# Kernel tuning notes

Measured on AMD Instinct MI355X. Metric: run time of the kernel, lower is better.

## Reference

```python
import jax, jax.numpy as jnp
import numpy as np

KERNEL = 3
BN_EPS = 1e-5


def setup_inputs() -> dict:
    key = jax.random.key(0)
    ks = jax.random.split(key, 4)
    B, C, H, W = 32, 256, 64, 64
    x = jax.random.normal(ks[0], (B, C, H, W), dtype=jnp.float32)
    conv_w = jax.random.normal(ks[1], (KERNEL * C, C), dtype=jnp.float32) * (1.0 / np.sqrt(C))
    bn_weight = jnp.ones((KERNEL * C,), dtype=jnp.float32)
    bn_bias = jnp.zeros((KERNEL * C,), dtype=jnp.float32)
    bn_mean = jnp.zeros((KERNEL * C,), dtype=jnp.float32)
    bn_var = jnp.ones((KERNEL * C,), dtype=jnp.float32)
    gamma = jax.random.normal(ks[2], (C, 1, 1), dtype=jnp.float32)
    beta = jnp.ones((C, 1, 1), dtype=jnp.float32)
    return {"x": x, "conv_w": conv_w, "bn_weight": bn_weight, "bn_bias": bn_bias,
            "bn_mean": bn_mean, "bn_var": bn_var, "gamma": gamma, "beta": beta}


def reference(x, conv_w, bn_weight, bn_bias, bn_mean, bn_var, gamma, beta):
    # x: (B, C, H, W)
    B, C, H, W = x.shape
    K = KERNEL
    # Filter generation: GAP -> 1x1 conv -> BN (inference stats) -> tanh
    g = x.mean(axis=(2, 3))                      # (B, C)
    y = jnp.einsum('bc,kc->bk', g, conv_w)       # (B, K*C)
    y = (y - bn_mean) * jax.lax.rsqrt(bn_var + BN_EPS) * bn_weight + bn_bias
    f = jnp.tanh(y).reshape(B, K, C)             # (B, K, C), tap k for channel c
    # Dynamic per-channel local filter along the CHANNEL axis with reflect pad.
    # Equivalent to the unfold path: out[b,c,h,w] = sum_k f[b,k,c] * x[b, reflect(c+k-1), h, w]
    xp = jnp.pad(x, ((0, 0), (K // 2, K // 2), (0, 0), (0, 0)), mode='reflect')
    out = f[:, 0, :, None, None] * xp[:, 0:C]
    for k in range(1, K):
        out = out + f[:, k, :, None, None] * xp[:, k:k + C]
    return out * gamma + x * beta
```

## Files before the change

### kernel.cpp

```cpp
#include <hip/hip_runtime.h>

#define NC 256
#define NB 32
#define HW 4096
#define HW4 1024
#define KC 768
#define BN_EPS 1e-5f
#define CG 32

typedef float f32x4 __attribute__((ext_vector_type(4)));

__global__ __launch_bounds__(256) void gap_kernel(const float* __restrict__ x,
                                                  float* __restrict__ g) {
    const int bc = blockIdx.x;
    const f32x4* xp = reinterpret_cast<const f32x4*>(x) + (size_t)bc * HW4;
    const int t = threadIdx.x;
    float s = 0.f;
#pragma unroll
    for (int k = 0; k < 4; ++k) {
        f32x4 v = xp[t + k * 256];
        s += (v.x + v.y) + (v.z + v.w);
    }
#pragma unroll
    for (int off = 32; off > 0; off >>= 1) s += __shfl_down(s, off, 64);
    __shared__ float warp_sums[4];
    const int lane = t & 63, w = t >> 6;
    if (lane == 0) warp_sums[w] = s;
    __syncthreads();
    if (t == 0) {
        float tot = (warp_sums[0] + warp_sums[1]) + (warp_sums[2] + warp_sums[3]);
        g[bc] = tot * (1.0f / HW);
    }
}

__global__ __launch_bounds__(256) void filt_kernel(const float* __restrict__ g,
                                                   const float* __restrict__ cw,
                                                   const float* __restrict__ bn_w,
                                                   const float* __restrict__ bn_b,
                                                   const float* __restrict__ bn_m,
                                                   const float* __restrict__ bn_v,
                                                   float* __restrict__ f) {
    const int b = blockIdx.y;
    const int t = threadIdx.x;
    __shared__ float gs[NC];
    gs[t] = g[b * NC + t];
    __syncthreads();
    const int wave = t >> 6, lane = t & 63;
    const f32x4 gv = reinterpret_cast<const f32x4*>(gs)[lane];
    const int row0 = blockIdx.x * 32 + wave * 8;
#pragma unroll
    for (int i = 0; i < 8; ++i) {
        const int j = row0 + i;
        const f32x4 wv = reinterpret_cast<const f32x4*>(cw + (size_t)j * NC)[lane];
        float s = fmaf(gv.x, wv.x, fmaf(gv.y, wv.y, fmaf(gv.z, wv.z, gv.w * wv.w)));
#pragma unroll
        for (int off = 32; off > 0; off >>= 1) s += __shfl_down(s, off, 64);
        if (lane == 0) {
            float yn = (s - bn_m[j]) * rsqrtf(bn_v[j] + BN_EPS) * bn_w[j] + bn_b[j];
            f[b * KC + j] = tanhf(yn);
        }
    }
}

__global__ __launch_bounds__(256) void apply_kernel(const float* __restrict__ x,
                                                    const float* __restrict__ f,
                                                    const float* __restrict__ gamma,
                                                    const float* __restrict__ beta,
                                                    float* __restrict__ out) {
    const int bid = blockIdx.x;
    const int cgp = bid & 7;
    const int b   = bid >> 3;
    const int t   = threadIdx.x;
    const int c0  = cgp * CG;

    __shared__ float f_s[3][CG];
    __shared__ float ga_s[CG], be_s[CG];
    {
        const float* fb = f + b * KC;
        if (t < 96)       f_s[t >> 5][t & 31] = fb[(t >> 5) * NC + c0 + (t & 31)];
        else if (t < 128) ga_s[t & 31] = gamma[c0 + (t & 31)];
        else if (t < 160) be_s[t & 31] = beta[c0 + (t & 31)];
    }

    const size_t bbase = (size_t)b * NC * HW4;
    const f32x4* x4 = reinterpret_cast<const f32x4*>(x) + bbase;
    f32x4* o4 = reinterpret_cast<f32x4*>(out) + bbase;

    f32x4 prv[4], cur[4], nxt[4];
#pragma unroll
    for (int j = 0; j < 4; ++j) cur[j] = x4[(size_t)c0 * HW4 + t + j * 256];
#pragma unroll
    for (int j = 0; j < 4; ++j) nxt[j] = x4[(size_t)(c0 + 1) * HW4 + t + j * 256];
    if (c0 == 0) {
#pragma unroll
        for (int j = 0; j < 4; ++j) prv[j] = nxt[j];
    } else {
#pragma unroll
        for (int j = 0; j < 4; ++j) prv[j] = x4[(size_t)(c0 - 1) * HW4 + t + j * 256];
    }
    __syncthreads();

#pragma unroll 2
    for (int ci = 0; ci < CG; ++ci) {
        const int c  = c0 + ci;
        const int cn = (c + 2 < NC) ? (c + 2) : (NC - 1);
        f32x4 nn[4];
#pragma unroll
        for (int j = 0; j < 4; ++j) nn[j] = x4[(size_t)cn * HW4 + t + j * 256];
        const float f0 = f_s[0][ci];
        const float f1 = f_s[1][ci];
        const float f2 = f_s[2][ci];
        const float ga = ga_s[ci];
        const float be = be_s[ci];
#pragma unroll
        for (int j = 0; j < 4; ++j) {
            const f32x4 xm = (c == 0) ? nxt[j] : prv[j];
            const f32x4 xq = (c == NC - 1) ? prv[j] : nxt[j];
            const f32x4 xc = cur[j];
            f32x4 r;
            r.x = fmaf(fmaf(f0, xm.x, fmaf(f1, xc.x, f2 * xq.x)), ga, xc.x * be);
            r.y = fmaf(fmaf(f0, xm.y, fmaf(f1, xc.y, f2 * xq.y)), ga, xc.y * be);
            r.z = fmaf(fmaf(f0, xm.z, fmaf(f1, xc.z, f2 * xq.z)), ga, xc.z * be);
            r.w = fmaf(fmaf(f0, xm.w, fmaf(f1, xc.w, f2 * xq.w)), ga, xc.w * be);
            o4[(size_t)c * HW4 + t + j * 256] = r;
        }
#pragma unroll
        for (int j = 0; j < 4; ++j) { prv[j] = cur[j]; cur[j] = nxt[j]; nxt[j] = nn[j]; }
    }
}

extern "C" void kernel_launch(void* const* d_in, const int* in_sizes, int n_in,
                              void* d_out, int out_size, void* d_ws, size_t ws_size,
                              hipStream_t stream) {
    const float* x     = (const float*)d_in[0];
    const float* cw    = (const float*)d_in[1];
    const float* bn_w  = (const float*)d_in[2];
    const float* bn_b  = (const float*)d_in[3];
    const float* bn_m  = (const float*)d_in[4];
    const float* bn_v  = (const float*)d_in[5];
    const float* gamma = (const float*)d_in[6];
    const float* beta  = (const float*)d_in[7];
    float* out = (float*)d_out;

    float* g = (float*)d_ws;
    float* f = g + NB * NC;

    gap_kernel<<<NB * NC, 256, 0, stream>>>(x, g);
    filt_kernel<<<dim3(24, NB), 256, 0, stream>>>(g, cw, bn_w, bn_b, bn_m, bn_v, f);
    apply_kernel<<<NB * (NC / CG), 256, 0, stream>>>(x, f, gamma, beta, out);
}
```

Baseline: 75.13 us.

## Fuse filter generation into the apply kernel and retile channel/spatial work

Removes the separate filter kernel: each apply block now computes its own 3x64 filter taps from the pooled means and the conv weights in a prologue, writing them to shared memory. The apply tiling changes to 64-channel groups with the spatial dimension split in two halves, so each thread holds 2 vectors instead of 4 and the grid keeps 256 blocks. This saves one kernel launch and the global round trip for the filter. In exchange every block redundantly reads part of the conv weight matrix (each batch recomputes its rows twice, once per half), and the filter matvec adds latency before streaming begins.

```diff
diff --git a/kernel.cpp b/kernel.cpp
--- a/kernel.cpp
+++ b/kernel.cpp
@@ -6,7 +6,7 @@
 #define HW4 1024
 #define KC 768
 #define BN_EPS 1e-5f
-#define CG 32
+#define CG 64
 
 typedef float f32x4 __attribute__((ext_vector_type(4)));
 
@@ -33,99 +33,95 @@
     }
 }
 
-__global__ __launch_bounds__(256) void filt_kernel(const float* __restrict__ g,
-                                                   const float* __restrict__ cw,
-                                                   const float* __restrict__ bn_w,
-                                                   const float* __restrict__ bn_b,
-                                                   const float* __restrict__ bn_m,
-                                                   const float* __restrict__ bn_v,
-                                                   float* __restrict__ f) {
-    const int b = blockIdx.y;
-    const int t = threadIdx.x;
+__global__ __launch_bounds__(256) void fused_kernel(
+    const float* __restrict__ x, const float* __restrict__ g,
+    const float* __restrict__ cw,
+    const float* __restrict__ bn_w, const float* __restrict__ bn_b,
+    const float* __restrict__ bn_m, const float* __restrict__ bn_v,
+    const float* __restrict__ gamma, const float* __restrict__ beta,
+    float* __restrict__ out) {
+    const int bid  = blockIdx.x;
+    const int half = bid & 1;
+    const int cgp  = (bid >> 1) & 3;
+    const int b    = bid >> 3;
+    const int t    = threadIdx.x;
+    const int wave = t >> 6, lane = t & 63;
+    const int c0   = cgp * CG;
+
     __shared__ float gs[NC];
     gs[t] = g[b * NC + t];
+    __shared__ float ga_s[CG], be_s[CG];
+    __shared__ float f_s[3][CG];
     __syncthreads();
-    const int wave = t >> 6, lane = t & 63;
-    const f32x4 gv = reinterpret_cast<const f32x4*>(gs)[lane];
-    const int row0 = blockIdx.x * 32 + wave * 8;
+
+    if (t < CG)            ga_s[t] = gamma[c0 + t];
+    else if (t < 2 * CG)   be_s[t - CG] = beta[c0 + t - CG];
+
+    {
+        const f32x4 gv = reinterpret_cast<const f32x4*>(gs)[lane];
 #pragma unroll
-    for (int i = 0; i < 8; ++i) {
-        const int j = row0 + i;
-        const f32x4 wv = reinterpret_cast<const f32x4*>(cw + (size_t)j * NC)[lane];
-        float s = fmaf(gv.x, wv.x, fmaf(gv.y, wv.y, fmaf(gv.z, wv.z, gv.w * wv.w)));
+        for (int r = 0; r < 48; ++r) {
+            const int rl = wave * 48 + r;
+            const int k  = rl >> 6;
+            const int ci = rl & 63;
+            const int j  = k * NC + c0 + ci;
+            const f32x4 wv = reinterpret_cast<const f32x4*>(cw + (size_t)j * NC)[lane];
+            float s = fmaf(gv.x, wv.x, fmaf(gv.y, wv.y, fmaf(gv.z, wv.z, gv.w * wv.w)));
 #pragma unroll
-        for (int off = 32; off > 0; off >>= 1) s += __shfl_down(s, off, 64);
-        if (lane == 0) {
-            float yn = (s - bn_m[j]) * rsqrtf(bn_v[j] + BN_EPS) * bn_w[j] + bn_b[j];
-            f[b * KC + j] = tanhf(yn);
+            for (int off = 32; off > 0; off >>= 1) s += __shfl_down(s, off, 64);
+            if (lane == 0) {
+                const float yn = (s - bn_m[j]) * rsqrtf(bn_v[j] + BN_EPS) * bn_w[j] + bn_b[j];
+                f_s[k][ci] = tanhf(yn);
+            }
         }
     }
-}
-
-__global__ __launch_bounds__(256) void apply_kernel(const float* __restrict__ x,
-                                                    const float* __restrict__ f,
-                                                    const float* __restrict__ gamma,
-                                                    const float* __restrict__ beta,
-                                                    float* __restrict__ out) {
-    const int bid = blockIdx.x;
-    const int cgp = bid & 7;
-    const int b   = bid >> 3;
-    const int t   = threadIdx.x;
-    const int c0  = cgp * CG;
-
-    __shared__ float f_s[3][CG];
-    __shared__ float ga_s[CG], be_s[CG];
-    {
-        const float* fb = f + b * KC;
-        if (t < 96)       f_s[t >> 5][t & 31] = fb[(t >> 5) * NC + c0 + (t & 31)];
-        else if (t < 128) ga_s[t & 31] = gamma[c0 + (t & 31)];
-        else if (t < 160) be_s[t & 31] = beta[c0 + (t & 31)];
-    }
+    __syncthreads();
 
     const size_t bbase = (size_t)b * NC * HW4;
     const f32x4* x4 = reinterpret_cast<const f32x4*>(x) + bbase;
     f32x4* o4 = reinterpret_cast<f32x4*>(out) + bbase;
+    const int col0 = half * 512 + t;
+    const int col1 = col0 + 256;
 
-    f32x4 prv[4], cur[4], nxt[4];
-#pragma unroll
-    for (int j = 0; j < 4; ++j) cur[j] = x4[(size_t)c0 * HW4 + t + j * 256];
-#pragma unroll
-    for (int j = 0; j < 4; ++j) nxt[j] = x4[(size_t)(c0 + 1) * HW4 + t + j * 256];
-    if (c0 == 0) {
-#pragma unroll
-        for (int j = 0; j < 4; ++j) prv[j] = nxt[j];
-    } else {
-#pragma unroll
-        for (int j = 0; j < 4; ++j) prv[j] = x4[(size_t)(c0 - 1) * HW4 + t + j * 256];
+    f32x4 prv0, prv1, cur0, cur1, nxt0, nxt1;
+    cur0 = x4[(size_t)c0 * HW4 + col0];
+    cur1 = x4[(size_t)c0 * HW4 + col1];
+    nxt0 = x4[(size_t)(c0 + 1) * HW4 + col0];
+    nxt1 = x4[(size_t)(c0 + 1) * HW4 + col1];
+    if (c0 == 0) { prv0 = nxt0; prv1 = nxt1; }
+    else {
+        prv0 = x4[(size_t)(c0 - 1) * HW4 + col0];
+        prv1 = x4[(size_t)(c0 - 1) * HW4 + col1];
     }
-    __syncthreads();
 
-#pragma unroll 2
+#pragma unroll 4
     for (int ci = 0; ci < CG; ++ci) {
         const int c  = c0 + ci;
         const int cn = (c + 2 < NC) ? (c + 2) : (NC - 1);
-        f32x4 nn[4];
-#pragma unroll
-        for (int j = 0; j < 4; ++j) nn[j] = x4[(size_t)cn * HW4 + t + j * 256];
+        f32x4 nn0 = x4[(size_t)cn * HW4 + col0];
+        f32x4 nn1 = x4[(size_t)cn * HW4 + col1];
         const float f0 = f_s[0][ci];
         const float f1 = f_s[1][ci];
         const float f2 = f_s[2][ci];
         const float ga = ga_s[ci];
         const float be = be_s[ci];
-#pragma unroll
-        for (int j = 0; j < 4; ++j) {
-            const f32x4 xm = (c == 0) ? nxt[j] : prv[j];
-            const f32x4 xq = (c == NC - 1) ? prv[j] : nxt[j];
-            const f32x4 xc = cur[j];
-            f32x4 r;
-            r.x = fmaf(fmaf(f0, xm.x, fmaf(f1, xc.x, f2 * xq.x)), ga, xc.x * be);
-            r.y = fmaf(fmaf(f0, xm.y, fmaf(f1, xc.y, f2 * xq.y)), ga, xc.y * be);
-            r.z = fmaf(fmaf(f0, xm.z, fmaf(f1, xc.z, f2 * xq.z)), ga, xc.z * be);
-            r.w = fmaf(fmaf(f0, xm.w, fmaf(f1, xc.w, f2 * xq.w)), ga, xc.w * be);
-            o4[(size_t)c * HW4 + t + j * 256] = r;
-        }
-#pragma unroll
-        for (int j = 0; j < 4; ++j) { prv[j] = cur[j]; cur[j] = nxt[j]; nxt[j] = nn[j]; }
+        const f32x4 xm0 = (c == 0) ? nxt0 : prv0;
+        const f32x4 xm1 = (c == 0) ? nxt1 : prv1;
+        const f32x4 xq0 = (c == NC - 1) ? prv0 : nxt0;
+        const f32x4 xq1 = (c == NC - 1) ? prv1 : nxt1;
+        f32x4 r0, r1;
+        r0.x = fmaf(fmaf(f0, xm0.x, fmaf(f1, cur0.x, f2 * xq0.x)), ga, cur0.x * be);
+        r0.y = fmaf(fmaf(f0, xm0.y, fmaf(f1, cur0.y, f2 * xq0.y)), ga, cur0.y * be);
+        r0.z = fmaf(fmaf(f0, xm0.z, fmaf(f1, cur0.z, f2 * xq0.z)), ga, cur0.z * be);
+        r0.w = fmaf(fmaf(f0, xm0.w, fmaf(f1, cur0.w, f2 * xq0.w)), ga, cur0.w * be);
+        r1.x = fmaf(fmaf(f0, xm1.x, fmaf(f1, cur1.x, f2 * xq1.x)), ga, cur1.x * be);
+        r1.y = fmaf(fmaf(f0, xm1.y, fmaf(f1, cur1.y, f2 * xq1.y)), ga, cur1.y * be);
+        r1.z = fmaf(fmaf(f0, xm1.z, fmaf(f1, cur1.z, f2 * xq1.z)), ga, cur1.z * be);
+        r1.w = fmaf(fmaf(f0, xm1.w, fmaf(f1, cur1.w, f2 * xq1.w)), ga, cur1.w * be);
+        o4[(size_t)c * HW4 + col0] = r0;
+        o4[(size_t)c * HW4 + col1] = r1;
+        prv0 = cur0; cur0 = nxt0; nxt0 = nn0;
+        prv1 = cur1; cur1 = nxt1; nxt1 = nn1;
     }
 }
 
@@ -143,9 +139,8 @@
     float* out = (float*)d_out;
 
     float* g = (float*)d_ws;
-    float* f = g + NB * NC;
 
     gap_kernel<<<NB * NC, 256, 0, stream>>>(x, g);
-    filt_kernel<<<dim3(24, NB), 256, 0, stream>>>(g, cw, bn_w, bn_b, bn_m, bn_v, f);
-    apply_kernel<<<NB * (NC / CG), 256, 0, stream>>>(x, f, gamma, beta, out);
+    fused_kernel<<<NB * (NC / CG) * 2, 256, 0, stream>>>(
+        x, g, cw, bn_w, bn_b, bn_m, bn_v, gamma, beta, out);
 }
```

After: 100.6 us. 1.34x slower.

## Fuse GAP, filter generation and apply into one kernel with per-batch spin barriers

Applied to the files above, without the earlier changes.

Replaces the three launches with a single 256-block kernel. Each block computes the channel means for its 32 channels, publishes them, then waits on a per-batch atomic counter until all 8 blocks of that batch are done. It then computes its own filter taps locally and applies the channel filter. This removes two launch gaps and the round trip of f through global memory, and x may stay partly in cache between the reduce and apply phases. The cost is a spin barrier that assumes all blocks are co-resident, an extra memset launch, and only 256 blocks doing the GAP work.

```diff
diff --git a/kernel.cpp b/kernel.cpp
--- a/kernel.cpp
+++ b/kernel.cpp
@@ -2,130 +2,152 @@
 
 #define NC 256
 #define NB 32
-#define HW 4096
 #define HW4 1024
 #define KC 768
 #define BN_EPS 1e-5f
-#define CG 32
 
 typedef float f32x4 __attribute__((ext_vector_type(4)));
 
-__global__ __launch_bounds__(256) void gap_kernel(const float* __restrict__ x,
-                                                  float* __restrict__ g) {
-    const int bc = blockIdx.x;
-    const f32x4* xp = reinterpret_cast<const f32x4*>(x) + (size_t)bc * HW4;
-    const int t = threadIdx.x;
-    float s = 0.f;
-#pragma unroll
-    for (int k = 0; k < 4; ++k) {
-        f32x4 v = xp[t + k * 256];
-        s += (v.x + v.y) + (v.z + v.w);
+__device__ __forceinline__ int spin_until(const int* p, int target) {
+    for (long it = 0; it < 4000000L; ++it) {
+        if (__hip_atomic_load(p, __ATOMIC_RELAXED, __HIP_MEMORY_SCOPE_AGENT) >= target) {
+            (void)__hip_atomic_load(p, __ATOMIC_ACQUIRE, __HIP_MEMORY_SCOPE_AGENT);
+            return 1;
+        }
+        __builtin_amdgcn_s_sleep(8);
     }
-#pragma unroll
-    for (int off = 32; off > 0; off >>= 1) s += __shfl_down(s, off, 64);
-    __shared__ float warp_sums[4];
-    const int lane = t & 63, w = t >> 6;
-    if (lane == 0) warp_sums[w] = s;
-    __syncthreads();
-    if (t == 0) {
-        float tot = (warp_sums[0] + warp_sums[1]) + (warp_sums[2] + warp_sums[3]);
-        g[bc] = tot * (1.0f / HW);
-    }
+    return 0;
 }
 
-__global__ __launch_bounds__(256) void filt_kernel(const float* __restrict__ g,
-                                                   const float* __restrict__ cw,
-                                                   const float* __restrict__ bn_w,
-                                                   const float* __restrict__ bn_b,
-                                                   const float* __restrict__ bn_m,
-                                                   const float* __restrict__ bn_v,
-                                                   float* __restrict__ f) {
-    const int b = blockIdx.y;
-    const int t = threadIdx.x;
+__global__ __launch_bounds__(256) void mega_kernel(
+    const float* __restrict__ x, const float* __restrict__ cw,
+    const float* __restrict__ bn_w, const float* __restrict__ bn_b,
+    const float* __restrict__ bn_m, const float* __restrict__ bn_v,
+    const float* __restrict__ gamma, const float* __restrict__ beta,
+    float* __restrict__ out, int* __restrict__ ctrs, float* __restrict__ g) {
+    const int bid   = blockIdx.x;
+    const int batch = bid >> 3;
+    const int slot  = bid & 7;
+    const int c0    = slot * 32;
+    const int t     = threadIdx.x;
+    const int wave  = t >> 6, lane = t & 63;
+
+    __shared__ float red[4][8];
+    __shared__ int ok_s;
     __shared__ float gs[NC];
-    gs[t] = g[b * NC + t];
-    __syncthreads();
-    const int wave = t >> 6, lane = t & 63;
-    const f32x4 gv = reinterpret_cast<const f32x4*>(gs)[lane];
-    const int row0 = blockIdx.x * 32 + wave * 8;
+    __shared__ float f_s[3][32];
+    __shared__ float ga_s[32], be_s[32];
+
+    int* gapd = &ctrs[batch * 32];
+    const f32x4* x4 = reinterpret_cast<const f32x4*>(x);
+    const size_t bbase = (size_t)batch * NC * HW4;
+
+    {
+        const f32x4* xp = x4 + bbase + (size_t)c0 * HW4;
+        for (int p0 = 0; p0 < 32; p0 += 8) {
+            float s[8];
 #pragma unroll
-    for (int i = 0; i < 8; ++i) {
-        const int j = row0 + i;
-        const f32x4 wv = reinterpret_cast<const f32x4*>(cw + (size_t)j * NC)[lane];
-        float s = fmaf(gv.x, wv.x, fmaf(gv.y, wv.y, fmaf(gv.z, wv.z, gv.w * wv.w)));
+            for (int p = 0; p < 8; ++p) {
+                const size_t pb = (size_t)(p0 + p) * HW4;
+                f32x4 a = xp[pb + t];
+                f32x4 b = xp[pb + t + 256];
+                f32x4 c = xp[pb + t + 512];
+                f32x4 d = xp[pb + t + 768];
+                s[p] = (((a.x + a.y) + (a.z + a.w)) + ((b.x + b.y) + (b.z + b.w))) +
+                       (((c.x + c.y) + (c.z + c.w)) + ((d.x + d.y) + (d.z + d.w)));
+            }
 #pragma unroll
-        for (int off = 32; off > 0; off >>= 1) s += __shfl_down(s, off, 64);
-        if (lane == 0) {
-            float yn = (s - bn_m[j]) * rsqrtf(bn_v[j] + BN_EPS) * bn_w[j] + bn_b[j];
-            f[b * KC + j] = tanhf(yn);
+            for (int p = 0; p < 8; ++p) {
+                float v = s[p];
+#pragma unroll
+                for (int off = 32; off > 0; off >>= 1) v += __shfl_down(v, off, 64);
+                if (lane == 0) red[wave][p] = v;
+            }
+            __syncthreads();
+            if (t < 8) {
+                float tot = (red[0][t] + red[1][t]) + (red[2][t] + red[3][t]);
+                g[batch * NC + c0 + p0 + t] = tot * (1.0f / 4096.0f);
+            }
+            __syncthreads();
         }
-    }
-}
-
-__global__ __launch_bounds__(256) void apply_kernel(const float* __restrict__ x,
-                                                    const float* __restrict__ f,
-                                                    const float* __restrict__ gamma,
-                                                    const float* __restrict__ beta,
-                                                    float* __restrict__ out) {
-    const int bid = blockIdx.x;
-    const int cgp = bid & 7;
-    const int b   = bid >> 3;
-    const int t   = threadIdx.x;
-    const int c0  = cgp * CG;
-
-    __shared__ float f_s[3][CG];
-    __shared__ float ga_s[CG], be_s[CG];
-    {
-        const float* fb = f + b * KC;
-        if (t < 96)       f_s[t >> 5][t & 31] = fb[(t >> 5) * NC + c0 + (t & 31)];
-        else if (t < 128) ga_s[t & 31] = gamma[c0 + (t & 31)];
-        else if (t < 160) be_s[t & 31] = beta[c0 + (t & 31)];
+        __threadfence();
+        __syncthreads();
+        if (t == 0) atomicAdd(gapd, 1);
     }
 
-    const size_t bbase = (size_t)b * NC * HW4;
-    const f32x4* x4 = reinterpret_cast<const f32x4*>(x) + bbase;
-    f32x4* o4 = reinterpret_cast<f32x4*>(out) + bbase;
+    if (t == 0) ok_s = spin_until(gapd, 8);
+    __syncthreads();
+    if (!ok_s) return;
+    gs[t] = __hip_atomic_load(&g[batch * NC + t], __ATOMIC_RELAXED,
+                              __HIP_MEMORY_SCOPE_AGENT);
+    if (t >= 192 && t < 224) ga_s[t - 192] = gamma[c0 + t - 192];
+    else if (t >= 224)       be_s[t - 224] = beta[c0 + t - 224];
+    __syncthreads();
 
-    f32x4 prv[4], cur[4], nxt[4];
+    {
+        const f32x4 gv = reinterpret_cast<const f32x4*>(gs)[lane];
+#pragma unroll 4
+        for (int r = 0; r < 24; ++r) {
+            const int rl = wave * 24 + r;
+            const int k  = rl >> 5;
+            const int ci = rl & 31;
+            const int j  = k * NC + c0 + ci;
+            const f32x4 wv = reinterpret_cast<const f32x4*>(cw + (size_t)j * NC)[lane];
+            float s = fmaf(gv.x, wv.x, fmaf(gv.y, wv.y, fmaf(gv.z, wv.z, gv.w * wv.w)));
 #pragma unroll
-    for (int j = 0; j < 4; ++j) cur[j] = x4[(size_t)c0 * HW4 + t + j * 256];
-#pragma unroll
-    for (int j = 0; j < 4; ++j) nxt[j] = x4[(size_t)(c0 + 1) * HW4 + t + j * 256];
-    if (c0 == 0) {
-#pragma unroll
-        for (int j = 0; j < 4; ++j) prv[j] = nxt[j];
-    } else {
-#pragma unroll
-        for (int j = 0; j < 4; ++j) prv[j] = x4[(size_t)(c0 - 1) * HW4 + t + j * 256];
+            for (int off = 32; off > 0; off >>= 1) s += __shfl_down(s, off, 64);
+            if (lane == 0) {
+                const float yn = (s - bn_m[j]) * rsqrtf(bn_v[j] + BN_EPS) * bn_w[j] + bn_b[j];
+                f_s[k][ci] = tanhf(yn);
+            }
+        }
     }
     __syncthreads();
 
+    {
+        const f32x4* xb = x4 + bbase;
+        f32x4* ob = reinterpret_cast<f32x4*>(out) + bbase;
+
+        f32x4 prv[4], cur[4], nxt[4];
+#pragma unroll
+        for (int j = 0; j < 4; ++j) cur[j] = xb[(size_t)c0 * HW4 + t + j * 256];
+#pragma unroll
+        for (int j = 0; j < 4; ++j) nxt[j] = xb[(size_t)(c0 + 1) * HW4 + t + j * 256];
+        if (c0 == 0) {
+#pragma unroll
+            for (int j = 0; j < 4; ++j) prv[j] = nxt[j];
+        } else {
+#pragma unroll
+            for (int j = 0; j < 4; ++j) prv[j] = xb[(size_t)(c0 - 1) * HW4 + t + j * 256];
+        }
+
 #pragma unroll 2
-    for (int ci = 0; ci < CG; ++ci) {
-        const int c  = c0 + ci;
-        const int cn = (c + 2 < NC) ? (c + 2) : (NC - 1);
-        f32x4 nn[4];
+        for (int ci = 0; ci < 32; ++ci) {
+            const int c  = c0 + ci;
+            const int cn = (c + 2 < NC) ? (c + 2) : (NC - 1);
+            f32x4 nn[4];
 #pragma unroll
-        for (int j = 0; j < 4; ++j) nn[j] = x4[(size_t)cn * HW4 + t + j * 256];
-        const float f0 = f_s[0][ci];
-        const float f1 = f_s[1][ci];
-        const float f2 = f_s[2][ci];
-        const float ga = ga_s[ci];
-        const float be = be_s[ci];
+            for (int j = 0; j < 4; ++j) nn[j] = xb[(size_t)cn * HW4 + t + j * 256];
+            const float f0 = f_s[0][ci];
+            const float f1 = f_s[1][ci];
+            const float f2 = f_s[2][ci];
+            const float ga = ga_s[ci];
+            const float be = be_s[ci];
 #pragma unroll
-        for (int j = 0; j < 4; ++j) {
-            const f32x4 xm = (c == 0) ? nxt[j] : prv[j];
-            const f32x4 xq = (c == NC - 1) ? prv[j] : nxt[j];
-            const f32x4 xc = cur[j];
-            f32x4 r;
-            r.x = fmaf(fmaf(f0, xm.x, fmaf(f1, xc.x, f2 * xq.x)), ga, xc.x * be);
-            r.y = fmaf(fmaf(f0, xm.y, fmaf(f1, xc.y, f2 * xq.y)), ga, xc.y * be);
-            r.z = fmaf(fmaf(f0, xm.z, fmaf(f1, xc.z, f2 * xq.z)), ga, xc.z * be);
-            r.w = fmaf(fmaf(f0, xm.w, fmaf(f1, xc.w, f2 * xq.w)), ga, xc.w * be);
-            o4[(size_t)c * HW4 + t + j * 256] = r;
+            for (int j = 0; j < 4; ++j) {
+                const f32x4 xm = (c == 0) ? nxt[j] : prv[j];
+                const f32x4 xq = (c == NC - 1) ? prv[j] : nxt[j];
+                const f32x4 xc = cur[j];
+                f32x4 r;
+                r.x = fmaf(fmaf(f0, xm.x, fmaf(f1, xc.x, f2 * xq.x)), ga, xc.x * be);
+                r.y = fmaf(fmaf(f0, xm.y, fmaf(f1, xc.y, f2 * xq.y)), ga, xc.y * be);
+                r.z = fmaf(fmaf(f0, xm.z, fmaf(f1, xc.z, f2 * xq.z)), ga, xc.z * be);
+                r.w = fmaf(fmaf(f0, xm.w, fmaf(f1, xc.w, f2 * xq.w)), ga, xc.w * be);
+                ob[(size_t)c * HW4 + t + j * 256] = r;
+            }
+#pragma unroll
+            for (int j = 0; j < 4; ++j) { prv[j] = cur[j]; cur[j] = nxt[j]; nxt[j] = nn[j]; }
         }
-#pragma unroll
-        for (int j = 0; j < 4; ++j) { prv[j] = cur[j]; cur[j] = nxt[j]; nxt[j] = nn[j]; }
     }
 }
 
@@ -142,10 +164,10 @@
     const float* beta  = (const float*)d_in[7];
     float* out = (float*)d_out;
 
-    float* g = (float*)d_ws;
-    float* f = g + NB * NC;
+    int*   ctrs = (int*)d_ws;
+    float* g    = (float*)((char*)d_ws + 8192);
 
-    gap_kernel<<<NB * NC, 256, 0, stream>>>(x, g);
-    filt_kernel<<<dim3(24, NB), 256, 0, stream>>>(g, cw, bn_w, bn_b, bn_m, bn_v, f);
-    apply_kernel<<<NB * (NC / CG), 256, 0, stream>>>(x, f, gamma, beta, out);
+    hipMemsetAsync(d_ws, 0, 8192, stream);
+    mega_kernel<<<256, 256, 0, stream>>>(
+        x, cw, bn_w, bn_b, bn_m, bn_v, gamma, beta, out, ctrs, g);
 }
```

After: 114.6 us. 52.5% more time.
